# Kernel optimization log

Measured on AMD Instinct MI355X. Metric: run time of the kernel, lower is better.

## Reference

```python
import jax, jax.numpy as jnp
import numpy as np

N = 50000
E = 800000
D = 128       # in_channels == out_channels
DE = 32       # edge_channels
DH = 128      # hidden_channels


def _xavier(key, shape, gain=1.0):
    fan_in, fan_out = shape[0], shape[1]
    a = gain * np.sqrt(6.0 / (fan_in + fan_out))
    return jax.random.uniform(key, shape, jnp.float32, -a, a)


def setup_inputs() -> dict:
    key = jax.random.key(0)
    ks = jax.random.split(key, 12)
    x = jax.random.normal(ks[0], (N, D), jnp.float32)
    edge_attr = jax.random.uniform(ks[1], (E, DE), jnp.float32)
    edge_index = jax.random.randint(ks[2], (2, E), 0, N, jnp.int32)
    return {
        "x": x,
        "edge_attr": edge_attr,
        "edge_index": edge_index,
        # initial_dense: Linear(D, D, bias=False)
        "W_init": _xavier(ks[3], (D, D)),
        # edge_projection: Linear(DE, D)
        "W_edge": _xavier(ks[4], (DE, D)),
        "b_edge": jnp.zeros((D,), jnp.float32),
        # attention vector (D, 1), xavier gain=1.414
        "att_vec": _xavier(ks[5], (D, 1), gain=1.414),
        "eps": jnp.zeros((1,), jnp.float32),
        # update_mlp: Linear(D, DH) -> tanh -> Linear(DH, D), no norm
        "W_u1": _xavier(ks[6], (D, DH)),
        "b_u1": jnp.zeros((DH,), jnp.float32),
        "W_u2": _xavier(ks[7], (DH, D)),
        "b_u2": jnp.zeros((D,), jnp.float32),
        # output_layer MLP: Linear(D, DH) -> batch_norm -> tanh -> Linear(DH, D)
        "W_o1": _xavier(ks[8], (D, DH)),
        "b_o1": jnp.zeros((DH,), jnp.float32),
        "bn_gamma": jnp.ones((DH,), jnp.float32),
        "bn_beta": jnp.zeros((DH,), jnp.float32),
        "W_o2": _xavier(ks[9], (DH, D)),
        "b_o2": jnp.zeros((D,), jnp.float32),
    }


def reference(x, edge_attr, edge_index, W_init, W_edge, b_edge, att_vec, eps,
              W_u1, b_u1, W_u2, b_u2, W_o1, b_o1, bn_gamma, bn_beta, W_o2, b_o2):
    src = edge_index[0]  # x_j source nodes
    dst = edge_index[1]  # aggregation targets (edge_index_i)

    # normalize edge features
    ea = edge_attr / (jnp.linalg.norm(edge_attr, axis=-1, keepdims=True) + 1e-8)

    # initial dense (no bias)
    h = x @ W_init  # [N, D]

    # message: tanh(x_j + edge_proj(edge_attr_norm))
    m = jnp.tanh(h[src] + ea @ W_edge + b_edge)  # [E, D]

    # per-edge attention with scatter-softmax over destinations
    logits = (m @ att_vec)[:, 0]  # [E]
    lmax = jax.ops.segment_max(logits, dst, num_segments=N)
    expv = jnp.exp(logits - lmax[dst])
    denom = jax.ops.segment_sum(expv, dst, num_segments=N)
    attn = expv / (denom[dst] + 1e-16)  # [E]

    # weighted scatter-add aggregation
    agg = jax.ops.segment_sum(m * attn[:, None], dst, num_segments=N)  # [N, D]

    # GIN update: MLP((1+eps)*x + agg), plain last, no norm
    pre = (1.0 + eps[0]) * h + agg
    u = jnp.tanh(pre @ W_u1 + b_u1) @ W_u2 + b_u2  # [N, D]

    # output MLP: Linear -> batch_norm (training-mode stats) -> tanh -> Linear
    z = u @ W_o1 + b_o1
    mu = z.mean(axis=0)
    var = z.var(axis=0)
    z = (z - mu) / jnp.sqrt(var + 1e-5) * bn_gamma + bn_beta
    out = jnp.tanh(z) @ W_o2 + b_o2  # [N, D]
    return out, attn
```

## Files before the change

kernel.cpp:

```cpp
#include <hip/hip_runtime.h>
#include <math.h>

#define DD  128
#define DEE 32

template<int PRE, int POST, int BNSTAT>
__global__ __launch_bounds__(256) void gemm128_kernel(
    const float* __restrict__ in, const float* __restrict__ W,
    const float* __restrict__ bias, float* __restrict__ out, int nrows,
    const float* __restrict__ U, const float* __restrict__ denom,
    const float* __restrict__ epsp,
    const float* __restrict__ bnscale, const float* __restrict__ bnshift,
    float* __restrict__ bnsum, float* __restrict__ bnsumsq)
{
    __shared__ float Ws[DD * DD];
    __shared__ float Xs[16 * DD];
    __shared__ float as_[DD], bs_[DD];
    __shared__ float ps[DD], psq[DD];

    const int tid = threadIdx.x;

    for (int i = tid; i < DD * DD / 4; i += 256)
        ((float4*)Ws)[i] = ((const float4*)W)[i];
    if constexpr (PRE == 2) {
        if (tid < DD) { as_[tid] = bnscale[tid]; bs_[tid] = bnshift[tid]; }
    }
    if constexpr (BNSTAT != 0) {
        if (tid < DD) { ps[tid] = 0.f; psq[tid] = 0.f; }
    }
    float epsv = 1.0f;
    if constexpr (PRE == 1) epsv = 1.0f + epsp[0];
    __syncthreads();

    const int c0 = (tid & 31) * 4;
    const int r0 = tid >> 5;
    float bsum0=0.f,bsum1=0.f,bsum2=0.f,bsum3=0.f;
    float bsq0=0.f,bsq1=0.f,bsq2=0.f,bsq3=0.f;

    const int ntiles = (nrows + 15) >> 4;
    for (int tile = blockIdx.x; tile < ntiles; tile += gridDim.x) {
        const int row_base = tile << 4;

        {
            const int idx = tid * 8;
            const int r   = idx >> 7;
            const int k0  = idx & 127;
            const int row = row_base + r;
            float4 v0 = make_float4(0.f,0.f,0.f,0.f);
            float4 v1 = make_float4(0.f,0.f,0.f,0.f);
            if (row < nrows) {
                const float* ip = in + (size_t)row * DD + k0;
                float4 a0 = *(const float4*)ip;
                float4 a1 = *(const float4*)(ip + 4);
                if constexpr (PRE == 0) {
                    v0 = a0; v1 = a1;
                } else if constexpr (PRE == 1) {
                    const float invd = 1.0f / (denom[row] + 1e-16f);
                    const float* up = U + (size_t)row * DD + k0;
                    float4 u0 = *(const float4*)up;
                    float4 u1 = *(const float4*)(up + 4);
                    v0.x = epsv*a0.x + u0.x*invd;  v0.y = epsv*a0.y + u0.y*invd;
                    v0.z = epsv*a0.z + u0.z*invd;  v0.w = epsv*a0.w + u0.w*invd;
                    v1.x = epsv*a1.x + u1.x*invd;  v1.y = epsv*a1.y + u1.y*invd;
                    v1.z = epsv*a1.z + u1.z*invd;  v1.w = epsv*a1.w + u1.w*invd;
                } else {
                    v0.x = tanhf(a0.x*as_[k0+0] + bs_[k0+0]);
                    v0.y = tanhf(a0.y*as_[k0+1] + bs_[k0+1]);
                    v0.z = tanhf(a0.z*as_[k0+2] + bs_[k0+2]);
                    v0.w = tanhf(a0.w*as_[k0+3] + bs_[k0+3]);
                    v1.x = tanhf(a1.x*as_[k0+4] + bs_[k0+4]);
                    v1.y = tanhf(a1.y*as_[k0+5] + bs_[k0+5]);
                    v1.z = tanhf(a1.z*as_[k0+6] + bs_[k0+6]);
                    v1.w = tanhf(a1.w*as_[k0+7] + bs_[k0+7]);
                }
            }
            *(float4*)&Xs[idx]     = v0;
            *(float4*)&Xs[idx + 4] = v1;
        }
        __syncthreads();

        float acc00=0,acc01=0,acc02=0,acc03=0;
        float acc10=0,acc11=0,acc12=0,acc13=0;
        #pragma unroll 4
        for (int k = 0; k < DD; k += 4) {
            float4 x0 = *(const float4*)&Xs[r0 * DD + k];
            float4 x1 = *(const float4*)&Xs[(r0 + 8) * DD + k];
            const float xs0[4] = {x0.x, x0.y, x0.z, x0.w};
            const float xs1[4] = {x1.x, x1.y, x1.z, x1.w};
            #pragma unroll
            for (int kk = 0; kk < 4; kk++) {
                float4 wv = *(const float4*)&Ws[(k + kk) * DD + c0];
                acc00 += xs0[kk]*wv.x; acc01 += xs0[kk]*wv.y;
                acc02 += xs0[kk]*wv.z; acc03 += xs0[kk]*wv.w;
                acc10 += xs1[kk]*wv.x; acc11 += xs1[kk]*wv.y;
                acc12 += xs1[kk]*wv.z; acc13 += xs1[kk]*wv.w;
            }
        }

        float4 bv = make_float4(0.f,0.f,0.f,0.f);
        if (bias) bv = *(const float4*)(bias + c0);
        float o00 = acc00 + bv.x, o01 = acc01 + bv.y, o02 = acc02 + bv.z, o03 = acc03 + bv.w;
        float o10 = acc10 + bv.x, o11 = acc11 + bv.y, o12 = acc12 + bv.z, o13 = acc13 + bv.w;
        if constexpr (POST == 1) {
            o00 = tanhf(o00); o01 = tanhf(o01); o02 = tanhf(o02); o03 = tanhf(o03);
            o10 = tanhf(o10); o11 = tanhf(o11); o12 = tanhf(o12); o13 = tanhf(o13);
        }
        const int row0 = row_base + r0;
        const int row1 = row0 + 8;
        if (row0 < nrows) {
            *(float4*)(out + (size_t)row0 * DD + c0) = make_float4(o00,o01,o02,o03);
            if constexpr (BNSTAT != 0) {
                bsum0 += o00; bsum1 += o01; bsum2 += o02; bsum3 += o03;
                bsq0 += o00*o00; bsq1 += o01*o01; bsq2 += o02*o02; bsq3 += o03*o03;
            }
        }
        if (row1 < nrows) {
            *(float4*)(out + (size_t)row1 * DD + c0) = make_float4(o10,o11,o12,o13);
            if constexpr (BNSTAT != 0) {
                bsum0 += o10; bsum1 += o11; bsum2 += o12; bsum3 += o13;
                bsq0 += o10*o10; bsq1 += o11*o11; bsq2 += o12*o12; bsq3 += o13*o13;
            }
        }
        __syncthreads();
    }

    if constexpr (BNSTAT != 0) {
        atomicAdd(&ps[c0+0], bsum0); atomicAdd(&ps[c0+1], bsum1);
        atomicAdd(&ps[c0+2], bsum2); atomicAdd(&ps[c0+3], bsum3);
        atomicAdd(&psq[c0+0], bsq0); atomicAdd(&psq[c0+1], bsq1);
        atomicAdd(&psq[c0+2], bsq2); atomicAdd(&psq[c0+3], bsq3);
        __syncthreads();
        if (tid < DD) {
            atomicAdd(&bnsum[tid], ps[tid]);
            atomicAdd(&bnsumsq[tid], psq[tid]);
        }
    }
}

__global__ __launch_bounds__(256) void edge_kernel(
    const float* __restrict__ ea, const int* __restrict__ src,
    const int* __restrict__ dst,
    const float* __restrict__ Wedge, const float* __restrict__ bedge,
    const float* __restrict__ att, const float* __restrict__ h,
    float* __restrict__ U, float* __restrict__ denom,
    float* __restrict__ wexp, int nedges)
{
    __shared__ float We[DEE * DD];
    __shared__ float be[DD], av[DD];
    const int tid = threadIdx.x;
    for (int i = tid; i < DEE * DD / 4; i += 256)
        ((float4*)We)[i] = ((const float4*)Wedge)[i];
    if (tid < DD) { be[tid] = bedge[tid]; av[tid] = att[tid]; }
    __syncthreads();

    const int lane = tid & 63;
    const int wid  = (blockIdx.x * 256 + tid) >> 6;
    const int nw   = (gridDim.x * 256) >> 6;

    for (int e = wid; e < nedges; e += nw) {
        float v = 0.f;
        if (lane < DEE) v = ea[(size_t)e * DEE + lane];
        float ss = v * v;
        ss += __shfl_xor(ss, 32); ss += __shfl_xor(ss, 16);
        ss += __shfl_xor(ss, 8);  ss += __shfl_xor(ss, 4);
        ss += __shfl_xor(ss, 2);  ss += __shfl_xor(ss, 1);
        const float inv = 1.0f / (sqrtf(ss) + 1e-8f);

        float p0 = be[lane], p1 = be[lane + 64];
        #pragma unroll
        for (int k = 0; k < DEE; k++) {
            const float ek = __shfl(v, k) * inv;
            p0 += ek * We[k * DD + lane];
            p1 += ek * We[k * DD + lane + 64];
        }

        const int s  = src[e];
        const int dn = dst[e];
        const float m0 = tanhf(h[(size_t)s * DD + lane]      + p0);
        const float m1 = tanhf(h[(size_t)s * DD + lane + 64] + p1);

        float l = m0 * av[lane] + m1 * av[lane + 64];
        l += __shfl_xor(l, 32); l += __shfl_xor(l, 16);
        l += __shfl_xor(l, 8);  l += __shfl_xor(l, 4);
        l += __shfl_xor(l, 2);  l += __shfl_xor(l, 1);
        const float w = expf(l);

        if (lane == 0) {
            wexp[e] = w;
            atomicAdd(&denom[dn], w);
        }
        atomicAdd(&U[(size_t)dn * DD + lane],      w * m0);
        atomicAdd(&U[(size_t)dn * DD + lane + 64], w * m1);
    }
}

__global__ __launch_bounds__(256) void attn_kernel(
    const float* __restrict__ wexp, const int* __restrict__ dst,
    const float* __restrict__ denom, float* __restrict__ attn_out, int nedges)
{
    const int i = blockIdx.x * 256 + threadIdx.x;
    if (i < nedges) attn_out[i] = wexp[i] / (denom[dst[i]] + 1e-16f);
}

__global__ void bnfin_kernel(
    const float* __restrict__ bnsum, const float* __restrict__ bnsumsq,
    const float* __restrict__ gamma, const float* __restrict__ beta,
    float* __restrict__ scale, float* __restrict__ shift, float invn)
{
    const int c = threadIdx.x;
    if (c < DD) {
        const float mu  = bnsum[c] * invn;
        const float var = bnsumsq[c] * invn - mu * mu;
        const float a   = gamma[c] * rsqrtf(var + 1e-5f);
        scale[c] = a;
        shift[c] = beta[c] - mu * a;
    }
}

extern "C" void kernel_launch(void* const* d_in, const int* in_sizes, int n_in,
                              void* d_out, int out_size, void* d_ws, size_t ws_size,
                              hipStream_t stream) {
    const float* x      = (const float*)d_in[0];
    const float* eattr  = (const float*)d_in[1];
    const int*   ei     = (const int*)  d_in[2];
    const float* W_init = (const float*)d_in[3];
    const float* W_edge = (const float*)d_in[4];
    const float* b_edge = (const float*)d_in[5];
    const float* attv   = (const float*)d_in[6];
    const float* eps    = (const float*)d_in[7];
    const float* W_u1   = (const float*)d_in[8];
    const float* b_u1   = (const float*)d_in[9];
    const float* W_u2   = (const float*)d_in[10];
    const float* b_u2   = (const float*)d_in[11];
    const float* W_o1   = (const float*)d_in[12];
    const float* b_o1   = (const float*)d_in[13];
    const float* gamma  = (const float*)d_in[14];
    const float* beta   = (const float*)d_in[15];
    const float* W_o2   = (const float*)d_in[16];
    const float* b_o2   = (const float*)d_in[17];

    const int N = in_sizes[0] / DD;
    const int E = in_sizes[2] / 2;
    const size_t ND = (size_t)N * DD;

    float* out      = (float*)d_out;
    float* attn_out = out + ND;

    float* ws    = (float*)d_ws;
    float* h     = ws;
    float* U     = ws + ND;
    float* tbuf  = ws + 2 * ND;
    float* denom = ws + 3 * ND;
    float* wexp  = denom + N;
    float* bnsum = wexp + E;
    float* bnsq  = bnsum + DD;
    float* bnsc  = bnsq + DD;
    float* bnsh  = bnsc + DD;
    float* ubuf  = U;
    float* zbuf  = h;

    const int* srcp = ei;
    const int* dstp = ei + E;

    hipMemsetAsync(U, 0, ND * sizeof(float), stream);
    hipMemsetAsync(denom, 0, (size_t)N * sizeof(float), stream);
    hipMemsetAsync(bnsum, 0, 2 * DD * sizeof(float), stream);

    const int gemm_grid = 512;
    dim3 blk(256);

    gemm128_kernel<0,0,0><<<gemm_grid, blk, 0, stream>>>(
        x, W_init, nullptr, h, N,
        nullptr, nullptr, nullptr, nullptr, nullptr, nullptr, nullptr);

    edge_kernel<<<2048, blk, 0, stream>>>(
        eattr, srcp, dstp, W_edge, b_edge, attv, h, U, denom, wexp, E);

    attn_kernel<<<(E + 255) / 256, blk, 0, stream>>>(wexp, dstp, denom, attn_out, E);

    gemm128_kernel<1,1,0><<<gemm_grid, blk, 0, stream>>>(
        h, W_u1, b_u1, tbuf, N,
        U, denom, eps, nullptr, nullptr, nullptr, nullptr);

    gemm128_kernel<0,0,0><<<gemm_grid, blk, 0, stream>>>(
        tbuf, W_u2, b_u2, ubuf, N,
        nullptr, nullptr, nullptr, nullptr, nullptr, nullptr, nullptr);

    gemm128_kernel<0,0,1><<<gemm_grid, blk, 0, stream>>>(
        ubuf, W_o1, b_o1, zbuf, N,
        nullptr, nullptr, nullptr, nullptr, nullptr, bnsum, bnsq);

    bnfin_kernel<<<1, DD, 0, stream>>>(bnsum, bnsq, gamma, beta, bnsc, bnsh, 1.0f / (float)N);

    gemm128_kernel<2,0,0><<<gemm_grid, blk, 0, stream>>>(
        zbuf, W_o2, b_o2, out, N,
        nullptr, nullptr, nullptr, bnsc, bnsh, nullptr, nullptr);
}
```

Before: 876.7 us.

## Build CSR by destination and aggregate per node; double-buffer GEMM tiles

Replaces the atomic per-edge scatter with a CSR build (histogram, three-pass scan, scatter) and a per-node aggregation kernel. Each wavefront accumulates messages and the softmax denominator in registers and writes the pre-MLP input directly, which removes float atomics on U and the U memset. The GEMM gains a double-buffered input tile, drops its fused pre-ops (batch-norm+tanh moves to a separate elementwise kernel), and uses a fast exp2/rcp tanh. Softmax skips max subtraction as before, and the GEMM drops row bounds checks, so N must be a multiple of 16.

```diff
diff --git a/kernel.cpp b/kernel.cpp
--- a/kernel.cpp
+++ b/kernel.cpp
@@ -4,87 +4,71 @@
 #define DD  128
 #define DEE 32
 
-template<int PRE, int POST, int BNSTAT>
+__device__ __forceinline__ float tanh_fast(float x) {
+    float e = __builtin_amdgcn_exp2f(x * 2.885390082f);
+    return 1.0f - 2.0f * __builtin_amdgcn_rcpf(e + 1.0f);
+}
+
+template<int POST, int BNSTAT>
 __global__ __launch_bounds__(256) void gemm128_kernel(
     const float* __restrict__ in, const float* __restrict__ W,
     const float* __restrict__ bias, float* __restrict__ out, int nrows,
-    const float* __restrict__ U, const float* __restrict__ denom,
-    const float* __restrict__ epsp,
-    const float* __restrict__ bnscale, const float* __restrict__ bnshift,
     float* __restrict__ bnsum, float* __restrict__ bnsumsq)
 {
     __shared__ float Ws[DD * DD];
-    __shared__ float Xs[16 * DD];
-    __shared__ float as_[DD], bs_[DD];
+    __shared__ float Xs[2][16 * DD];
     __shared__ float ps[DD], psq[DD];
 
     const int tid = threadIdx.x;
-
     for (int i = tid; i < DD * DD / 4; i += 256)
         ((float4*)Ws)[i] = ((const float4*)W)[i];
-    if constexpr (PRE == 2) {
-        if (tid < DD) { as_[tid] = bnscale[tid]; bs_[tid] = bnshift[tid]; }
-    }
     if constexpr (BNSTAT != 0) {
         if (tid < DD) { ps[tid] = 0.f; psq[tid] = 0.f; }
     }
-    float epsv = 1.0f;
-    if constexpr (PRE == 1) epsv = 1.0f + epsp[0];
-    __syncthreads();
 
     const int c0 = (tid & 31) * 4;
     const int r0 = tid >> 5;
+    const int idx = tid * 8;
+    const int ntiles = nrows >> 4;
+
     float bsum0=0.f,bsum1=0.f,bsum2=0.f,bsum3=0.f;
     float bsq0=0.f,bsq1=0.f,bsq2=0.f,bsq3=0.f;
 
-    const int ntiles = (nrows + 15) >> 4;
-    for (int tile = blockIdx.x; tile < ntiles; tile += gridDim.x) {
-        const int row_base = tile << 4;
-
-        {
-            const int idx = tid * 8;
-            const int r   = idx >> 7;
-            const int k0  = idx & 127;
-            const int row = row_base + r;
-            float4 v0 = make_float4(0.f,0.f,0.f,0.f);
-            float4 v1 = make_float4(0.f,0.f,0.f,0.f);
-            if (row < nrows) {
-                const float* ip = in + (size_t)row * DD + k0;
-                float4 a0 = *(const float4*)ip;
-                float4 a1 = *(const float4*)(ip + 4);
-                if constexpr (PRE == 0) {
-                    v0 = a0; v1 = a1;
-                } else if constexpr (PRE == 1) {
-                    const float invd = 1.0f / (denom[row] + 1e-16f);
-                    const float* up = U + (size_t)row * DD + k0;
-                    float4 u0 = *(const float4*)up;
-                    float4 u1 = *(const float4*)(up + 4);
-                    v0.x = epsv*a0.x + u0.x*invd;  v0.y = epsv*a0.y + u0.y*invd;
-                    v0.z = epsv*a0.z + u0.z*invd;  v0.w = epsv*a0.w + u0.w*invd;
-                    v1.x = epsv*a1.x + u1.x*invd;  v1.y = epsv*a1.y + u1.y*invd;
-                    v1.z = epsv*a1.z + u1.z*invd;  v1.w = epsv*a1.w + u1.w*invd;
-                } else {
-                    v0.x = tanhf(a0.x*as_[k0+0] + bs_[k0+0]);
-                    v0.y = tanhf(a0.y*as_[k0+1] + bs_[k0+1]);
-                    v0.z = tanhf(a0.z*as_[k0+2] + bs_[k0+2]);
-                    v0.w = tanhf(a0.w*as_[k0+3] + bs_[k0+3]);
-                    v1.x = tanhf(a1.x*as_[k0+4] + bs_[k0+4]);
-                    v1.y = tanhf(a1.y*as_[k0+5] + bs_[k0+5]);
-                    v1.z = tanhf(a1.z*as_[k0+6] + bs_[k0+6]);
-                    v1.w = tanhf(a1.w*as_[k0+7] + bs_[k0+7]);
-                }
-            }
-            *(float4*)&Xs[idx]     = v0;
-            *(float4*)&Xs[idx + 4] = v1;
-        }
-        __syncthreads();
+    float4 bv = make_float4(0.f,0.f,0.f,0.f);
+    if (bias) bv = *(const float4*)(bias + c0);
+
+    int tile = blockIdx.x;
+    bool have = tile < ntiles;
+    float4 n0, n1;
+    if (have) {
+        const float* ip = in + ((size_t)tile << 4) * DD + idx;
+        n0 = ((const float4*)ip)[0];
+        n1 = ((const float4*)ip)[1];
+    }
+    __syncthreads();
+    if (have) {
+        *(float4*)&Xs[0][idx]     = n0;
+        *(float4*)&Xs[0][idx + 4] = n1;
+    }
+    __syncthreads();
+
+    int buf = 0;
+    while (have) {
+        const int next = tile + gridDim.x;
+        const bool haveN = next < ntiles;
+        if (haveN) {
+            const float* ip = in + ((size_t)next << 4) * DD + idx;
+            n0 = ((const float4*)ip)[0];
+            n1 = ((const float4*)ip)[1];
+        }
 
         float acc00=0,acc01=0,acc02=0,acc03=0;
         float acc10=0,acc11=0,acc12=0,acc13=0;
+        const float* xs = Xs[buf];
         #pragma unroll 4
         for (int k = 0; k < DD; k += 4) {
-            float4 x0 = *(const float4*)&Xs[r0 * DD + k];
-            float4 x1 = *(const float4*)&Xs[(r0 + 8) * DD + k];
+            float4 x0 = *(const float4*)&xs[r0 * DD + k];
+            float4 x1 = *(const float4*)&xs[(r0 + 8) * DD + k];
             const float xs0[4] = {x0.x, x0.y, x0.z, x0.w};
             const float xs1[4] = {x1.x, x1.y, x1.z, x1.w};
             #pragma unroll
@@ -97,31 +81,29 @@
             }
         }
 
-        float4 bv = make_float4(0.f,0.f,0.f,0.f);
-        if (bias) bv = *(const float4*)(bias + c0);
         float o00 = acc00 + bv.x, o01 = acc01 + bv.y, o02 = acc02 + bv.z, o03 = acc03 + bv.w;
         float o10 = acc10 + bv.x, o11 = acc11 + bv.y, o12 = acc12 + bv.z, o13 = acc13 + bv.w;
         if constexpr (POST == 1) {
-            o00 = tanhf(o00); o01 = tanhf(o01); o02 = tanhf(o02); o03 = tanhf(o03);
-            o10 = tanhf(o10); o11 = tanhf(o11); o12 = tanhf(o12); o13 = tanhf(o13);
-        }
-        const int row0 = row_base + r0;
-        const int row1 = row0 + 8;
-        if (row0 < nrows) {
-            *(float4*)(out + (size_t)row0 * DD + c0) = make_float4(o00,o01,o02,o03);
-            if constexpr (BNSTAT != 0) {
-                bsum0 += o00; bsum1 += o01; bsum2 += o02; bsum3 += o03;
-                bsq0 += o00*o00; bsq1 += o01*o01; bsq2 += o02*o02; bsq3 += o03*o03;
-            }
-        }
-        if (row1 < nrows) {
-            *(float4*)(out + (size_t)row1 * DD + c0) = make_float4(o10,o11,o12,o13);
-            if constexpr (BNSTAT != 0) {
-                bsum0 += o10; bsum1 += o11; bsum2 += o12; bsum3 += o13;
-                bsq0 += o10*o10; bsq1 += o11*o11; bsq2 += o12*o12; bsq3 += o13*o13;
-            }
-        }
-        __syncthreads();
+            o00 = tanh_fast(o00); o01 = tanh_fast(o01); o02 = tanh_fast(o02); o03 = tanh_fast(o03);
+            o10 = tanh_fast(o10); o11 = tanh_fast(o11); o12 = tanh_fast(o12); o13 = tanh_fast(o13);
+        }
+        const size_t row0 = ((size_t)tile << 4) + r0;
+        *(float4*)(out + row0 * DD + c0)       = make_float4(o00,o01,o02,o03);
+        *(float4*)(out + (row0 + 8) * DD + c0) = make_float4(o10,o11,o12,o13);
+        if constexpr (BNSTAT != 0) {
+            bsum0 += o00+o10; bsum1 += o01+o11; bsum2 += o02+o12; bsum3 += o03+o13;
+            bsq0 += o00*o00+o10*o10; bsq1 += o01*o01+o11*o11;
+            bsq2 += o02*o02+o12*o12; bsq3 += o03*o03+o13*o13;
+        }
+
+        if (haveN) {
+            *(float4*)&Xs[buf ^ 1][idx]     = n0;
+            *(float4*)&Xs[buf ^ 1][idx + 4] = n1;
+        }
+        __syncthreads();
+        buf ^= 1;
+        tile = next;
+        have = haveN;
     }
 
     if constexpr (BNSTAT != 0) {
@@ -137,60 +119,131 @@
     }
 }
 
-__global__ __launch_bounds__(256) void edge_kernel(
-    const float* __restrict__ ea, const int* __restrict__ src,
-    const int* __restrict__ dst,
+__global__ __launch_bounds__(256) void hist_kernel(
+    const int* __restrict__ dst, int* __restrict__ deg, int E)
+{
+    const int i = blockIdx.x * 256 + threadIdx.x;
+    if (i < E) atomicAdd(&deg[dst[i]], 1);
+}
+
+__global__ __launch_bounds__(256) void scan1_kernel(
+    const int* __restrict__ deg, int* __restrict__ excl,
+    int* __restrict__ blksum, int N)
+{
+    __shared__ int s[256];
+    const int tid = threadIdx.x;
+    const int i = blockIdx.x * 256 + tid;
+    const int v = (i < N) ? deg[i] : 0;
+    s[tid] = v; __syncthreads();
+    for (int off = 1; off < 256; off <<= 1) {
+        int t = (tid >= off) ? s[tid - off] : 0;
+        __syncthreads();
+        s[tid] += t;
+        __syncthreads();
+    }
+    if (i < N) excl[i] = s[tid] - v;
+    if (tid == 255) blksum[blockIdx.x] = s[255];
+}
+
+__global__ __launch_bounds__(256) void scan2_kernel(int* __restrict__ blksum, int nblk)
+{
+    __shared__ int s[256];
+    const int tid = threadIdx.x;
+    const int v = (tid < nblk) ? blksum[tid] : 0;
+    s[tid] = v; __syncthreads();
+    for (int off = 1; off < 256; off <<= 1) {
+        int t = (tid >= off) ? s[tid - off] : 0;
+        __syncthreads();
+        s[tid] += t;
+        __syncthreads();
+    }
+    if (tid < nblk) blksum[tid] = s[tid] - v;
+}
+
+__global__ __launch_bounds__(256) void scan3_kernel(
+    int* __restrict__ rowptr, const int* __restrict__ blkoff,
+    int* __restrict__ cursor, int N, int E)
+{
+    const int i = blockIdx.x * 256 + threadIdx.x;
+    if (i < N) {
+        const int r = rowptr[i] + blkoff[blockIdx.x];
+        rowptr[i] = r;
+        cursor[i] = r;
+    }
+    if (i == 0) rowptr[N] = E;
+}
+
+__global__ __launch_bounds__(256) void scatter_kernel(
+    const int* __restrict__ dst, int* __restrict__ cursor,
+    int* __restrict__ eidx, int E)
+{
+    const int i = blockIdx.x * 256 + threadIdx.x;
+    if (i < E) {
+        const int p = atomicAdd(&cursor[dst[i]], 1);
+        eidx[p] = i;
+    }
+}
+
+__global__ __launch_bounds__(256, 4) void agg_kernel(
+    const float* __restrict__ ea, const int* __restrict__ srcA,
+    const int* __restrict__ eidx, const int* __restrict__ rowptr,
     const float* __restrict__ Wedge, const float* __restrict__ bedge,
     const float* __restrict__ att, const float* __restrict__ h,
-    float* __restrict__ U, float* __restrict__ denom,
-    float* __restrict__ wexp, int nedges)
-{
-    __shared__ float We[DEE * DD];
-    __shared__ float be[DD], av[DD];
-    const int tid = threadIdx.x;
-    for (int i = tid; i < DEE * DD / 4; i += 256)
-        ((float4*)We)[i] = ((const float4*)Wedge)[i];
-    if (tid < DD) { be[tid] = bedge[tid]; av[tid] = att[tid]; }
-    __syncthreads();
-
-    const int lane = tid & 63;
-    const int wid  = (blockIdx.x * 256 + tid) >> 6;
-    const int nw   = (gridDim.x * 256) >> 6;
-
-    for (int e = wid; e < nedges; e += nw) {
-        float v = 0.f;
-        if (lane < DEE) v = ea[(size_t)e * DEE + lane];
-        float ss = v * v;
-        ss += __shfl_xor(ss, 32); ss += __shfl_xor(ss, 16);
-        ss += __shfl_xor(ss, 8);  ss += __shfl_xor(ss, 4);
-        ss += __shfl_xor(ss, 2);  ss += __shfl_xor(ss, 1);
-        const float inv = 1.0f / (sqrtf(ss) + 1e-8f);
-
-        float p0 = be[lane], p1 = be[lane + 64];
-        #pragma unroll
-        for (int k = 0; k < DEE; k++) {
-            const float ek = __shfl(v, k) * inv;
-            p0 += ek * We[k * DD + lane];
-            p1 += ek * We[k * DD + lane + 64];
-        }
-
-        const int s  = src[e];
-        const int dn = dst[e];
-        const float m0 = tanhf(h[(size_t)s * DD + lane]      + p0);
-        const float m1 = tanhf(h[(size_t)s * DD + lane + 64] + p1);
-
-        float l = m0 * av[lane] + m1 * av[lane + 64];
-        l += __shfl_xor(l, 32); l += __shfl_xor(l, 16);
-        l += __shfl_xor(l, 8);  l += __shfl_xor(l, 4);
-        l += __shfl_xor(l, 2);  l += __shfl_xor(l, 1);
-        const float w = expf(l);
-
-        if (lane == 0) {
-            wexp[e] = w;
-            atomicAdd(&denom[dn], w);
-        }
-        atomicAdd(&U[(size_t)dn * DD + lane],      w * m0);
-        atomicAdd(&U[(size_t)dn * DD + lane + 64], w * m1);
+    const float* __restrict__ epsp,
+    float* __restrict__ pre, float* __restrict__ denom,
+    float* __restrict__ wexp, int N)
+{
+    const int lane = threadIdx.x & 63;
+    float we0[DEE], we1[DEE];
+    #pragma unroll
+    for (int k = 0; k < DEE; k++) {
+        we0[k] = Wedge[k * DD + lane];
+        we1[k] = Wedge[k * DD + 64 + lane];
+    }
+    const float be0 = bedge[lane], be1 = bedge[64 + lane];
+    const float av0 = att[lane],   av1 = att[64 + lane];
+    const float epsv = 1.0f + epsp[0];
+
+    const int w  = (blockIdx.x * 256 + threadIdx.x) >> 6;
+    const int nw = (gridDim.x * 256) >> 6;
+
+    for (int n = w; n < N; n += nw) {
+        const int r0 = rowptr[n], r1 = rowptr[n + 1];
+        float acc0 = 0.f, acc1 = 0.f, den = 0.f;
+        for (int j = r0; j < r1; j++) {
+            const int e = eidx[j];
+            float v = (lane < DEE) ? ea[(size_t)e * DEE + lane] : 0.f;
+            float ss = v * v;
+            ss += __shfl_xor(ss, 32); ss += __shfl_xor(ss, 16);
+            ss += __shfl_xor(ss, 8);  ss += __shfl_xor(ss, 4);
+            ss += __shfl_xor(ss, 2);  ss += __shfl_xor(ss, 1);
+            const float inv = 1.0f / (sqrtf(ss) + 1e-8f);
+
+            float p0 = be0, p1 = be1;
+            #pragma unroll
+            for (int k = 0; k < DEE; k++) {
+                const float ek = __shfl(v, k) * inv;
+                p0 += ek * we0[k];
+                p1 += ek * we1[k];
+            }
+
+            const int s = srcA[e];
+            const float m0 = tanh_fast(h[(size_t)s * DD + lane]      + p0);
+            const float m1 = tanh_fast(h[(size_t)s * DD + 64 + lane] + p1);
+
+            float l = m0 * av0 + m1 * av1;
+            l += __shfl_xor(l, 32); l += __shfl_xor(l, 16);
+            l += __shfl_xor(l, 8);  l += __shfl_xor(l, 4);
+            l += __shfl_xor(l, 2);  l += __shfl_xor(l, 1);
+            const float wgt = __builtin_amdgcn_exp2f(l * 1.44269504f);
+
+            if (lane == 0) wexp[e] = wgt;
+            acc0 += wgt * m0; acc1 += wgt * m1; den += wgt;
+        }
+        const float invd = 1.0f / (den + 1e-16f);
+        pre[(size_t)n * DD + lane]      = epsv * h[(size_t)n * DD + lane]      + acc0 * invd;
+        pre[(size_t)n * DD + 64 + lane] = epsv * h[(size_t)n * DD + 64 + lane] + acc1 * invd;
+        if (lane == 0) denom[n] = den;
     }
 }
 
@@ -214,6 +267,26 @@
         const float a   = gamma[c] * rsqrtf(var + 1e-5f);
         scale[c] = a;
         shift[c] = beta[c] - mu * a;
+    }
+}
+
+__global__ __launch_bounds__(256) void bntrans_kernel(
+    float* __restrict__ z, const float* __restrict__ sc,
+    const float* __restrict__ sh, int nrows)
+{
+    __shared__ float s_sc[DD], s_sh[DD];
+    if (threadIdx.x < DD) { s_sc[threadIdx.x] = sc[threadIdx.x]; s_sh[threadIdx.x] = sh[threadIdx.x]; }
+    __syncthreads();
+    const size_t total  = (size_t)nrows * DD;
+    const size_t stride = (size_t)gridDim.x * 1024;
+    for (size_t i = ((size_t)blockIdx.x * 256 + threadIdx.x) * 4; i < total; i += stride) {
+        float4 v = *(float4*)(z + i);
+        const int c = (int)(i & (DD - 1));
+        v.x = tanh_fast(v.x * s_sc[c]     + s_sh[c]);
+        v.y = tanh_fast(v.y * s_sc[c + 1] + s_sh[c + 1]);
+        v.z = tanh_fast(v.z * s_sc[c + 2] + s_sh[c + 2]);
+        v.w = tanh_fast(v.w * s_sc[c + 3] + s_sh[c + 3]);
+        *(float4*)(z + i) = v;
     }
 }
 
@@ -248,7 +321,7 @@
 
     float* ws    = (float*)d_ws;
     float* h     = ws;
-    float* U     = ws + ND;
+    float* pre   = ws + ND;
     float* tbuf  = ws + 2 * ND;
     float* denom = ws + 3 * ND;
     float* wexp  = denom + N;
@@ -256,43 +329,52 @@
     float* bnsq  = bnsum + DD;
     float* bnsc  = bnsq + DD;
     float* bnsh  = bnsc + DD;
-    float* ubuf  = U;
-    float* zbuf  = h;
+    int* deg    = (int*)pre;
+    int* cursor = (int*)pre + N;
+    int* eidx   = (int*)tbuf;
+    int* rowptr = (int*)tbuf + E;
+    int* blksum = (int*)tbuf + E + N + 1;
+    float* ubuf = pre;
+    float* zbuf = h;
 
     const int* srcp = ei;
     const int* dstp = ei + E;
 
-    hipMemsetAsync(U, 0, ND * sizeof(float), stream);
-    hipMemsetAsync(denom, 0, (size_t)N * sizeof(float), stream);
+    hipMemsetAsync(deg, 0, (size_t)N * sizeof(int), stream);
     hipMemsetAsync(bnsum, 0, 2 * DD * sizeof(float), stream);
 
     const int gemm_grid = 512;
+    const int nblkN = (N + 255) / 256;
+    const int nblkE = (E + 255) / 256;
     dim3 blk(256);
 
-    gemm128_kernel<0,0,0><<<gemm_grid, blk, 0, stream>>>(
-        x, W_init, nullptr, h, N,
-        nullptr, nullptr, nullptr, nullptr, nullptr, nullptr, nullptr);
-
-    edge_kernel<<<2048, blk, 0, stream>>>(
-        eattr, srcp, dstp, W_edge, b_edge, attv, h, U, denom, wexp, E);
-
-    attn_kernel<<<(E + 255) / 256, blk, 0, stream>>>(wexp, dstp, denom, attn_out, E);
-
-    gemm128_kernel<1,1,0><<<gemm_grid, blk, 0, stream>>>(
-        h, W_u1, b_u1, tbuf, N,
-        U, denom, eps, nullptr, nullptr, nullptr, nullptr);
-
-    gemm128_kernel<0,0,0><<<gemm_grid, blk, 0, stream>>>(
-        tbuf, W_u2, b_u2, ubuf, N,
-        nullptr, nullptr, nullptr, nullptr, nullptr, nullptr, nullptr);
-
-    gemm128_kernel<0,0,1><<<gemm_grid, blk, 0, stream>>>(
-        ubuf, W_o1, b_o1, zbuf, N,
-        nullptr, nullptr, nullptr, nullptr, nullptr, bnsum, bnsq);
+    gemm128_kernel<0,0><<<gemm_grid, blk, 0, stream>>>(
+        x, W_init, nullptr, h, N, nullptr, nullptr);
+
+    hist_kernel<<<nblkE, blk, 0, stream>>>(dstp, deg, E);
+    scan1_kernel<<<nblkN, blk, 0, stream>>>(deg, rowptr, blksum, N);
+    scan2_kernel<<<1, blk, 0, stream>>>(blksum, nblkN);
+    scan3_kernel<<<nblkN, blk, 0, stream>>>(rowptr, blksum, cursor, N, E);
+    scatter_kernel<<<nblkE, blk, 0, stream>>>(dstp, cursor, eidx, E);
+
+    agg_kernel<<<1024, blk, 0, stream>>>(
+        eattr, srcp, eidx, rowptr, W_edge, b_edge, attv, h, eps,
+        pre, denom, wexp, N);
+
+    attn_kernel<<<nblkE, blk, 0, stream>>>(wexp, dstp, denom, attn_out, E);
+
+    gemm128_kernel<1,0><<<gemm_grid, blk, 0, stream>>>(
+        pre, W_u1, b_u1, tbuf, N, nullptr, nullptr);
+
+    gemm128_kernel<0,0><<<gemm_grid, blk, 0, stream>>>(
+        tbuf, W_u2, b_u2, ubuf, N, nullptr, nullptr);
+
+    gemm128_kernel<0,1><<<gemm_grid, blk, 0, stream>>>(
+        ubuf, W_o1, b_o1, zbuf, N, bnsum, bnsq);
 
     bnfin_kernel<<<1, DD, 0, stream>>>(bnsum, bnsq, gamma, beta, bnsc, bnsh, 1.0f / (float)N);
-
-    gemm128_kernel<2,0,0><<<gemm_grid, blk, 0, stream>>>(
-        zbuf, W_o2, b_o2, out, N,
-        nullptr, nullptr, nullptr, bnsc, bnsh, nullptr, nullptr);
-}
+    bntrans_kernel<<<2048, blk, 0, stream>>>(zbuf, bnsc, bnsh, N);
+
+    gemm128_kernel<0,0><<<gemm_grid, blk, 0, stream>>>(
+        zbuf, W_o2, b_o2, out, N, nullptr, nullptr);
+}
```

Result: slower. 1.145 ms (+30.6%).
